# Optimization experiments

Hardware: AMD Instinct MI355X
Metric: run time of the kernel (lower is better)

## Reference

```python
import jax, jax.numpy as jnp
import numpy as np

N = 50000   # nodes
E = 800000  # edges (avg degree 16)
G = 32      # graphs in batch
IN = 128; HID = 64; H = 2; C = 16
NEG_SLOPE = 0.2
BN_EPS = 1e-5


def setup_inputs() -> dict:
    key = jax.random.key(0)
    ks = jax.random.split(key, 16)
    def rn(k, shape, scale=0.1):
        return jax.random.normal(k, shape, jnp.float32) * scale
    return {
        "feat": jax.random.normal(ks[0], (N, IN), jnp.float32),
        "W0": rn(ks[1], (IN, H * HID)),
        "attn0": rn(ks[2], (H, HID)),
        "W1": rn(ks[3], (H * HID, H * HID)),
        "attn1": rn(ks[4], (H, HID)),
        "W2": rn(ks[5], (H * HID, H * HID)),
        "attn2": rn(ks[6], (H, HID)),
        "Wf": rn(ks[7], (H * HID, H * C)),
        "attnf": rn(ks[8], (H, C)),
        "mlp_w1": rn(ks[9], (C, C)),
        "mlp_gamma": jnp.ones((C,), jnp.float32),
        "mlp_beta": jnp.zeros((C,), jnp.float32),
        "mlp_w2": rn(ks[10], (C, C)),
        "src": jax.random.randint(ks[11], (E,), 0, N, jnp.int32),
        "dst": jax.random.randint(ks[12], (E,), 0, N, jnp.int32),
        "node_graph": jnp.sort(jax.random.randint(ks[13], (N,), 0, G, jnp.int32)),
        "num_graphs": G,
    }


def gatv2_layer(h, src, dst, W, attn, act):
    """DGL GATv2Conv with share_weights=True, bias=False, residual=False."""
    n = h.shape[0]
    nh, d = attn.shape
    z = (h @ W).reshape(n, nh, d)                      # [N,H,D]
    zs = z[src]                                        # [E,H,D] gather (src)
    e = jax.nn.leaky_relu(zs + z[dst], NEG_SLOPE)      # [E,H,D]
    score = jnp.einsum('ehd,hd->eh', e, attn)          # [E,H]
    # edge softmax over incoming edges of dst (shift-invariant max trick)
    m = jax.lax.stop_gradient(jax.ops.segment_max(score, dst, num_segments=n))
    a = jnp.exp(score - m[dst])
    denom = jax.ops.segment_sum(a, dst, num_segments=n)[dst]
    alpha = a / jnp.where(denom == 0, 1.0, denom)      # [E,H]
    out = jax.ops.segment_sum(alpha[..., None] * zs, dst, num_segments=n)  # [N,H,D]
    return act(out) if act is not None else out


def reference(feat, W0, attn0, W1, attn1, W2, attn2, Wf, attnf,
              mlp_w1, mlp_gamma, mlp_beta, mlp_w2,
              src, dst, node_graph, num_graphs):
    relu = jax.nn.relu
    n = feat.shape[0]
    h = gatv2_layer(feat, src, dst, W0, attn0, relu).reshape(n, -1)
    h = gatv2_layer(h, src, dst, W1, attn1, relu).reshape(n, -1)
    h = gatv2_layer(h, src, dst, W2, attn2, relu).reshape(n, -1)
    logits = gatv2_layer(h, src, dst, Wf, attnf, None).mean(axis=1)  # [N,C]
    pooled = jax.ops.segment_sum(logits, node_graph, num_segments=num_graphs)  # [G,C]
    # MLP: relu(batchnorm(lin0(x))) -> lin1 (training-mode batch stats, biased var)
    h1 = pooled @ mlp_w1
    mu = h1.mean(axis=0)
    var = h1.var(axis=0)
    h1 = (h1 - mu) / jnp.sqrt(var + BN_EPS) * mlp_gamma + mlp_beta
    out = relu(h1) @ mlp_w2
    return jax.nn.log_softmax(out, axis=-1)
```

## Files before the change

### kernel.cpp

```cpp
#include <hip/hip_runtime.h>
#include <hip/hip_bf16.h>
#include <hip/hip_fp16.h>
#include <math.h>

#define NN 50000
#define EE 800000
#define GG 32
#define HD 64
#define NHEAD 2
#define CCLS 16
#define NEG_SLOPE 0.2f
#define BN_EPS 1e-5f
#define LOG2E 1.4426950408889634f
#define STRIDE 64

typedef unsigned int u32;
typedef _Float16 hv2 __attribute__((ext_vector_type(2)));
typedef __fp16   cv2 __attribute__((ext_vector_type(2)));

__device__ __forceinline__ hv2 bch2(u32 u) { union { u32 u; hv2 h; } c; c.u = u; return c.h; }
__device__ __forceinline__ u32 pkrtz(float a, float b) {
    cv2 r = __builtin_amdgcn_cvt_pkrtz(a, b);
    union { cv2 h; u32 u; } c; c.h = r; return c.u;
}
__device__ __forceinline__ hv2 h2max(hv2 a, hv2 b) {
    return __builtin_elementwise_max(a, b);
}
__device__ __forceinline__ float fdot2(hv2 a, hv2 b, float c) {
#if __has_builtin(__builtin_amdgcn_fdot2)
    union { hv2 h; cv2 c2; } ua, ub;
    ua.h = a; ub.h = b;
    return __builtin_amdgcn_fdot2(ua.c2, ub.c2, c, false);
#else
    return fmaf((float)a[0], (float)b[0], fmaf((float)a[1], (float)b[1], c));
#endif
}


template<int KOUT, int RPT, bool F16IN>
__device__ __forceinline__ void gemm_body(const void* __restrict__ hv,
                                          const float* __restrict__ W,
                                          u32* __restrict__ z, int n, int blk) {
    constexpr int CT = KOUT / 8;
    constexpr int RT = 256 / CT;
    constexpr int BR = RT * RPT;
    constexpr int WSTR = KOUT + 4;
    __shared__ __align__(16) u32 WpD[64 * WSTR];
    __shared__ __align__(16) uint4 hsU4[BR * 17];
    int t = threadIdx.x;
    int row0 = blk * BR;

    for (int i = t; i < 64 * (KOUT / 4); i += 256) {
        int k2 = i / (KOUT / 4), cq = i % (KOUT / 4);
        float4 wa = ((const float4*)W)[(2 * k2) * (KOUT / 4) + cq];
        float4 wb = ((const float4*)W)[(2 * k2 + 1) * (KOUT / 4) + cq];
        uint4 d;
        d.x = pkrtz(wa.x, wb.x); d.y = pkrtz(wa.y, wb.y);
        d.z = pkrtz(wa.z, wb.z); d.w = pkrtz(wa.w, wb.w);
        ((uint4*)&WpD[k2 * WSTR])[cq] = d;
    }
    for (int i = t; i < BR * 16; i += 256) {
        int r = i >> 4, c16 = i & 15;
        int gr = row0 + r;
        uint4 u = {0, 0, 0, 0};
        if (gr < n) {
            if (F16IN) {
                u = ((const uint4*)hv)[(size_t)gr * 16 + c16];
            } else {
                float4 f0 = ((const float4*)hv)[(size_t)gr * 32 + 2 * c16];
                float4 f1 = ((const float4*)hv)[(size_t)gr * 32 + 2 * c16 + 1];
                u.x = pkrtz(f0.x, f0.y); u.y = pkrtz(f0.z, f0.w);
                u.z = pkrtz(f1.x, f1.y); u.w = pkrtz(f1.z, f1.w);
            }
        }
        hsU4[r * 17 + c16] = u;
    }
    __syncthreads();

    int tc = t % CT, tr = t / CT;
    float acc[RPT][8];
    #pragma unroll
    for (int i = 0; i < RPT; i++)
        #pragma unroll
        for (int c = 0; c < 8; c++) acc[i][c] = 0.f;

    for (int kq = 0; kq < 16; kq++) {
        uint4 a4[RPT];
        #pragma unroll
        for (int i = 0; i < RPT; i++) a4[i] = hsU4[(tr * RPT + i) * 17 + kq];
        #pragma unroll
        for (int j = 0; j < 4; j++) {
            const u32* wrow = &WpD[(4 * kq + j) * WSTR + tc * 8];
            uint4 wa = *(const uint4*)wrow;
            uint4 wb = *(const uint4*)(wrow + 4);
            u32 wd[8] = {wa.x, wa.y, wa.z, wa.w, wb.x, wb.y, wb.z, wb.w};
            #pragma unroll
            for (int i = 0; i < RPT; i++) {
                u32 av[4] = {a4[i].x, a4[i].y, a4[i].z, a4[i].w};
                hv2 a2 = bch2(av[j]);
                #pragma unroll
                for (int c = 0; c < 8; c++)
                    acc[i][c] = fdot2(a2, bch2(wd[c]), acc[i][c]);
            }
        }
    }
    #pragma unroll
    for (int i = 0; i < RPT; i++) {
        int gr = row0 + tr * RPT + i;
        if (gr < n) {
            uint4 p;
            p.x = pkrtz(acc[i][0], acc[i][1]);
            p.y = pkrtz(acc[i][2], acc[i][3]);
            p.z = pkrtz(acc[i][4], acc[i][5]);
            p.w = pkrtz(acc[i][6], acc[i][7]);
            ((uint4*)z)[(size_t)gr * (KOUT / 8) + tc] = p;
        }
    }
}

template<int KOUT, int RPT, bool F16IN>
__global__ __launch_bounds__(256) void gemm_kernel(const void* __restrict__ hv,
                                                   const float* __restrict__ W,
                                                   u32* __restrict__ z, int n) {
    gemm_body<KOUT, RPT, F16IN>(hv, W, z, n, blockIdx.x);
}


#define GB0 782
#define SB0 782

__global__ __launch_bounds__(256) void gemm0_scatter_kernel(const float* __restrict__ feat,
                                                            const float* __restrict__ W,
                                                            u32* __restrict__ z,
                                                            const int* __restrict__ src,
                                                            const int* __restrict__ dst,
                                                            int* __restrict__ cursor,
                                                            int* __restrict__ csr_src) {
    if (blockIdx.x < GB0) {
        gemm_body<128, 4, false>(feat, W, z, NN, blockIdx.x);
    } else {
        int b = blockIdx.x - GB0;
        int e0 = b * 1024 + threadIdx.x;
        #pragma unroll
        for (int q = 0; q < 4; q++) {
            int e = e0 + q * 256;
            if (e < EE) {
                int d = dst[e];
                int s = src[e];
                int p = atomicAdd(&cursor[d], 1);
                csr_src[d * STRIDE + p] = s;
            }
        }
    }
}


__global__ __launch_bounds__(256) void edge_kernel(const u32* __restrict__ z,
                                                   const float* __restrict__ attn,
                                                   const int* __restrict__ cursor,
                                                   const int* __restrict__ csr_src,
                                                   u32* __restrict__ out, int n) {
    int wave = blockIdx.x * 4 + (threadIdx.x >> 6);
    int lane = threadIdx.x & 63;
    if (wave >= n) return;
    int i = wave;
    int slot = lane >> 3;
    int q8 = lane & 7;
    const uint4* zr = (const uint4*)z;

    size_t rowi = (size_t)i * 16 + q8 * 2;
    uint4 zua = zr[rowi], zub = zr[rowi + 1];
    hv2 zd[8] = {bch2(zua.x), bch2(zua.y), bch2(zua.z), bch2(zua.w),
                 bch2(zub.x), bch2(zub.y), bch2(zub.z), bch2(zub.w)};
    const float4* af = (const float4*)attn;
    float4 a0 = af[q8 * 4 + 0], a1 = af[q8 * 4 + 1];
    float4 a2 = af[q8 * 4 + 2], a3 = af[q8 * 4 + 3];
    hv2 ah[8] = {bch2(pkrtz(a0.x * LOG2E, a0.y * LOG2E)),
                 bch2(pkrtz(a0.z * LOG2E, a0.w * LOG2E)),
                 bch2(pkrtz(a1.x * LOG2E, a1.y * LOG2E)),
                 bch2(pkrtz(a1.z * LOG2E, a1.w * LOG2E)),
                 bch2(pkrtz(a2.x * LOG2E, a2.y * LOG2E)),
                 bch2(pkrtz(a2.z * LOG2E, a2.w * LOG2E)),
                 bch2(pkrtz(a3.x * LOG2E, a3.y * LOG2E)),
                 bch2(pkrtz(a3.z * LOG2E, a3.w * LOG2E))};
    const hv2 slope2 = {(_Float16)NEG_SLOPE, (_Float16)NEG_SLOPE};

    int deg = cursor[i];
    const int* ep = csr_src + i * STRIDE;

    float s = 0.f;
    float accf[16];
    #pragma unroll
    for (int j = 0; j < 16; j++) accf[j] = 0.f;

    for (int k = 0; k < deg; k += 8) {
        int kk = k + slot;
        bool valid = kk < deg;
        int sid = valid ? ep[kk] : i;
        size_t rs = (size_t)sid * 16 + q8 * 2;
        uint4 sa = zr[rs], sb = zr[rs + 1];
        hv2 zs[8] = {bch2(sa.x), bch2(sa.y), bch2(sa.z), bch2(sa.w),
                     bch2(sb.x), bch2(sb.y), bch2(sb.z), bch2(sb.w)};
        float sc = 0.f;
        #pragma unroll
        for (int j = 0; j < 8; j++) {
            hv2 x = zs[j] + zd[j];
            x = h2max(x, x * slope2);
            sc = fdot2(x, ah[j], sc);
        }
        sc += __shfl_xor(sc, 2, 64);
        sc += __shfl_xor(sc, 1, 64);
        float p = valid ? exp2f(sc) : 0.f;
        s += p;
        #pragma unroll
        for (int j = 0; j < 8; j++) {
            accf[2 * j]     = fmaf(p, (float)zs[j][0], accf[2 * j]);
            accf[2 * j + 1] = fmaf(p, (float)zs[j][1], accf[2 * j + 1]);
        }
    }

    #pragma unroll
    for (int off = 8; off <= 32; off <<= 1) {
        s += __shfl_xor(s, off, 64);
        #pragma unroll
        for (int j = 0; j < 16; j++) accf[j] += __shfl_xor(accf[j], off, 64);
    }

    if (slot == 0) {
        float inv = s > 0.f ? 1.f / s : 0.f;
        float o[16];
        #pragma unroll
        for (int j = 0; j < 16; j++) o[j] = fmaxf(accf[j] * inv, 0.f);
        uint4 pa, pb;
        pa.x = pkrtz(o[0], o[1]);   pa.y = pkrtz(o[2], o[3]);
        pa.z = pkrtz(o[4], o[5]);   pa.w = pkrtz(o[6], o[7]);
        pb.x = pkrtz(o[8], o[9]);   pb.y = pkrtz(o[10], o[11]);
        pb.z = pkrtz(o[12], o[13]); pb.w = pkrtz(o[14], o[15]);
        ((uint4*)out)[rowi] = pa;
        ((uint4*)out)[rowi + 1] = pb;
    }
}


__global__ __launch_bounds__(256) void edge_final_kernel(const u32* __restrict__ z,
                                                         const float* __restrict__ attn,
                                                         const int* __restrict__ cursor,
                                                         const int* __restrict__ csr_src,
                                                         float* __restrict__ logits, int n) {
    int wave = blockIdx.x * 4 + (threadIdx.x >> 6);
    int lane = threadIdx.x & 63;
    int iv = wave * 2 + (lane >> 5);
    bool mine = iv < n;
    int i = mine ? iv : (n - 1);
    int hl = lane & 31;
    int j = hl >> 3;
    int d8 = hl & 7;
    const uint2* zr = (const uint2*)z;
    uint2 zu = zr[(size_t)i * 8 + d8];
    hv2 zd0 = bch2(zu.x), zd1 = bch2(zu.y);
    float4 av = ((const float4*)attn)[d8];
    hv2 ah0 = bch2(pkrtz(av.x * LOG2E, av.y * LOG2E));
    hv2 ah1 = bch2(pkrtz(av.z * LOG2E, av.w * LOG2E));
    const hv2 slope2 = {(_Float16)NEG_SLOPE, (_Float16)NEG_SLOPE};
    int deg = cursor[i];
    const int* ep = csr_src + i * STRIDE;

    float s = 0.f;
    float accf[4] = {0.f, 0.f, 0.f, 0.f};
    for (int k = 0; k < deg; k += 4) {
        int kk = k + j;
        bool valid = kk < deg;
        int sid = valid ? ep[kk] : i;
        uint2 su = zr[(size_t)sid * 8 + d8];
        hv2 zs0 = bch2(su.x), zs1 = bch2(su.y);
        hv2 x;
        float sc = 0.f;
        x = zs0 + zd0; x = h2max(x, x * slope2); sc = fdot2(x, ah0, sc);
        x = zs1 + zd1; x = h2max(x, x * slope2); sc = fdot2(x, ah1, sc);
        sc += __shfl_xor(sc, 1, 64);
        sc += __shfl_xor(sc, 2, 64);
        float p = valid ? exp2f(sc) : 0.f;
        s += p;
        accf[0] = fmaf(p, (float)zs0[0], accf[0]);
        accf[1] = fmaf(p, (float)zs0[1], accf[1]);
        accf[2] = fmaf(p, (float)zs1[0], accf[2]);
        accf[3] = fmaf(p, (float)zs1[1], accf[3]);
    }
    #pragma unroll
    for (int off = 8; off <= 16; off <<= 1) {
        s += __shfl_xor(s, off, 64);
        #pragma unroll
        for (int jj = 0; jj < 4; jj++) accf[jj] += __shfl_xor(accf[jj], off, 64);
    }
    float inv = s > 0.f ? 1.f / s : 0.f;
    float4 o;
    o.x = accf[0] * inv; o.y = accf[1] * inv; o.z = accf[2] * inv; o.w = accf[3] * inv;
    o.x = 0.5f * (o.x + __shfl_xor(o.x, 4, 64));
    o.y = 0.5f * (o.y + __shfl_xor(o.y, 4, 64));
    o.z = 0.5f * (o.z + __shfl_xor(o.z, 4, 64));
    o.w = 0.5f * (o.w + __shfl_xor(o.w, 4, 64));
    if (mine && j == 0 && (hl & 4) == 0)
        ((float4*)logits)[i * 4 + (hl & 3)] = o;
}


__global__ __launch_bounds__(256) void pool_kernel(const float* __restrict__ logits,
                                                   const int* __restrict__ node_graph,
                                                   float* __restrict__ pooled) {
    int t = threadIdx.x;
    int c = t & 15;
    int ci = t >> 4;
    int start = blockIdx.x * 1024 + ci * 64;
    float acc = 0.f;
    int gcur = -1;
    for (int j = 0; j < 64; j++) {
        int node = start + j;
        if (node >= NN) break;
        int g = node_graph[node];
        if (g != gcur) {
            if (gcur >= 0) atomicAdd(&pooled[gcur * 16 + c], acc);
            gcur = g; acc = 0.f;
        }
        acc += logits[node * 16 + c];
    }
    if (gcur >= 0) atomicAdd(&pooled[gcur * 16 + c], acc);
}


__global__ __launch_bounds__(512) void mlp_kernel(const float* __restrict__ pooled,
                                                  const float* __restrict__ w1,
                                                  const float* __restrict__ gamma,
                                                  const float* __restrict__ beta,
                                                  const float* __restrict__ w2,
                                                  float* __restrict__ out) {
    __shared__ float P[GG * CCLS], H1[GG * CCLS], H2[GG * CCLS], O[GG * CCLS];
    __shared__ float mu[CCLS], rstd[CCLS], rowm[GG], rowl[GG];
    int t = threadIdx.x;
    int r = t >> 4, c = t & 15;
    if (t < GG * CCLS) P[t] = pooled[t];
    __syncthreads();
    if (t < GG * CCLS) {
        float s = 0.f;
        for (int k = 0; k < 16; k++) s += P[r * 16 + k] * w1[k * 16 + c];
        H1[t] = s;
    }
    __syncthreads();
    if (t < CCLS) {
        float s = 0.f;
        for (int rr = 0; rr < GG; rr++) s += H1[rr * 16 + t];
        float mn = s / GG;
        float s2 = 0.f;
        for (int rr = 0; rr < GG; rr++) { float d = H1[rr * 16 + t] - mn; s2 += d * d; }
        mu[t] = mn; rstd[t] = rsqrtf(s2 / GG + BN_EPS);
    }
    __syncthreads();
    if (t < GG * CCLS) {
        float v = (H1[t] - mu[c]) * rstd[c] * gamma[c] + beta[c];
        H2[t] = fmaxf(v, 0.f);
    }
    __syncthreads();
    if (t < GG * CCLS) {
        float s = 0.f;
        for (int k = 0; k < 16; k++) s += H2[r * 16 + k] * w2[k * 16 + c];
        O[t] = s;
    }
    __syncthreads();
    if (t < GG) {
        float mx = -INFINITY;
        for (int k = 0; k < 16; k++) mx = fmaxf(mx, O[t * 16 + k]);
        float l = 0.f;
        for (int k = 0; k < 16; k++) l += __expf(O[t * 16 + k] - mx);
        rowm[t] = mx; rowl[t] = logf(l);
    }
    __syncthreads();
    if (t < GG * CCLS) out[t] = O[t] - rowm[r] - rowl[r];
}


extern "C" void kernel_launch(void* const* d_in, const int* in_sizes, int n_in,
                              void* d_out, int out_size, void* d_ws, size_t ws_size,
                              hipStream_t stream) {
    const float* feat     = (const float*)d_in[0];
    const float* W0       = (const float*)d_in[1];
    const float* attn0    = (const float*)d_in[2];
    const float* W1       = (const float*)d_in[3];
    const float* attn1    = (const float*)d_in[4];
    const float* W2       = (const float*)d_in[5];
    const float* attn2    = (const float*)d_in[6];
    const float* Wf       = (const float*)d_in[7];
    const float* attnf    = (const float*)d_in[8];
    const float* mlp_w1   = (const float*)d_in[9];
    const float* mlp_g    = (const float*)d_in[10];
    const float* mlp_b    = (const float*)d_in[11];
    const float* mlp_w2   = (const float*)d_in[12];
    const int*   src      = (const int*)d_in[13];
    const int*   dst      = (const int*)d_in[14];
    const int*   ngraph   = (const int*)d_in[15];
    float* out = (float*)d_out;

    char* ws = (char*)d_ws;
    size_t off = 0;
    auto alloc = [&](size_t bytes) {
        void* p = ws + off;
        off = (off + bytes + 255) & ~(size_t)255;
        return p;
    };
    u32* z      = (u32*)alloc((size_t)NN * 64 * sizeof(u32));
    u32* hb0    = (u32*)alloc((size_t)NN * 64 * sizeof(u32));
    u32* hb1    = (u32*)alloc((size_t)NN * 64 * sizeof(u32));
    float* logits = (float*)alloc((size_t)NN * 16 * sizeof(float));
    float* pooled = (float*)alloc(GG * CCLS * sizeof(float));
    int* cursor   = (int*)alloc(NN * sizeof(int));
    int* csr_src  = (int*)alloc((size_t)NN * STRIDE * sizeof(int));

    hipMemsetAsync(cursor, 0, NN * sizeof(int), stream);
    hipMemsetAsync(pooled, 0, GG * CCLS * sizeof(float), stream);

    int edge_grid = (NN + 3) / 4;
    int edgef_grid = (NN + 7) / 8;
    int gemm_grid = (NN + 63) / 64;

    gemm0_scatter_kernel<<<GB0 + SB0, 256, 0, stream>>>(feat, W0, z, src, dst,
                                                        cursor, csr_src);
    edge_kernel<<<edge_grid, 256, 0, stream>>>(z, attn0, cursor, csr_src, hb0, NN);

    gemm_kernel<128, 4, true><<<gemm_grid, 256, 0, stream>>>(hb0, W1, z, NN);
    edge_kernel<<<edge_grid, 256, 0, stream>>>(z, attn1, cursor, csr_src, hb1, NN);

    gemm_kernel<128, 4, true><<<gemm_grid, 256, 0, stream>>>(hb1, W2, z, NN);
    edge_kernel<<<edge_grid, 256, 0, stream>>>(z, attn2, cursor, csr_src, hb0, NN);

    gemm_kernel<32, 1, true><<<gemm_grid, 256, 0, stream>>>(hb0, Wf, z, NN);
    edge_final_kernel<<<edgef_grid, 256, 0, stream>>>(z, attnf, cursor, csr_src, logits, NN);

    pool_kernel<<<(NN + 1023) / 1024, 256, 0, stream>>>(logits, ngraph, pooled);
    mlp_kernel<<<1, 512, 0, stream>>>(pooled, mlp_w1, mlp_g, mlp_b, mlp_w2, out);
}
```

Measured before the change: 427.2 us.

## Split gemm0/scatter kernels, pad weight LDS layout, prefetch next edge batch

Splits the fused first GEMM + CSR scatter kernel into two separate launches, and restructures the scatter to load all four dst/src pairs before issuing atomics. Pads the KOUT=128 weight tile in LDS with an extra 4-word gap every 32 words to reduce bank conflicts on the uint4 reads. In the edge kernel, the gather of the next batch of 8 neighbor rows is software-prefetched while the current batch is being computed, to hide gather latency at the cost of extra registers. Splitting the fused kernel removes the concurrency between the GEMM and the scatter and adds one launch.

```diff
diff --git a/kernel.cpp b/kernel.cpp
--- a/kernel.cpp
+++ b/kernel.cpp
@@ -37,6 +37,30 @@
 }
 
 
+__global__ __launch_bounds__(256) void scatter_kernel(const int* __restrict__ src,
+                                                      const int* __restrict__ dst,
+                                                      int* __restrict__ cursor,
+                                                      int* __restrict__ csr_src) {
+    int e0 = blockIdx.x * 1024 + threadIdx.x;
+    int d[4], s[4];
+    bool v[4];
+    #pragma unroll
+    for (int q = 0; q < 4; q++) {
+        int e = e0 + q * 256;
+        v[q] = e < EE;
+        d[q] = v[q] ? dst[e] : 0;
+        s[q] = v[q] ? src[e] : 0;
+    }
+    #pragma unroll
+    for (int q = 0; q < 4; q++) {
+        if (v[q]) {
+            int p = atomicAdd(&cursor[d[q]], 1);
+            csr_src[d[q] * STRIDE + p] = s[q];
+        }
+    }
+}
+
+
 template<int KOUT, int RPT, bool F16IN>
 __device__ __forceinline__ void gemm_body(const void* __restrict__ hv,
                                           const float* __restrict__ W,
@@ -44,7 +68,7 @@
     constexpr int CT = KOUT / 8;
     constexpr int RT = 256 / CT;
     constexpr int BR = RT * RPT;
-    constexpr int WSTR = KOUT + 4;
+    constexpr int WSTR = (KOUT == 128) ? 140 : (KOUT + 4);
     __shared__ __align__(16) u32 WpD[64 * WSTR];
     __shared__ __align__(16) uint4 hsU4[BR * 17];
     int t = threadIdx.x;
@@ -57,7 +81,7 @@
         uint4 d;
         d.x = pkrtz(wa.x, wb.x); d.y = pkrtz(wa.y, wb.y);
         d.z = pkrtz(wa.z, wb.z); d.w = pkrtz(wa.w, wb.w);
-        ((uint4*)&WpD[k2 * WSTR])[cq] = d;
+        *(uint4*)&WpD[k2 * WSTR + 4 * cq + ((cq >> 3) << 2)] = d;
     }
     for (int i = t; i < BR * 16; i += 256) {
         int r = i >> 4, c16 = i & 15;
@@ -90,7 +114,7 @@
         for (int i = 0; i < RPT; i++) a4[i] = hsU4[(tr * RPT + i) * 17 + kq];
         #pragma unroll
         for (int j = 0; j < 4; j++) {
-            const u32* wrow = &WpD[(4 * kq + j) * WSTR + tc * 8];
+            const u32* wrow = &WpD[(4 * kq + j) * WSTR + tc * 8 + ((tc >> 2) << 2)];
             uint4 wa = *(const uint4*)wrow;
             uint4 wb = *(const uint4*)(wrow + 4);
             u32 wd[8] = {wa.x, wa.y, wa.z, wa.w, wb.x, wb.y, wb.z, wb.w};
@@ -123,35 +147,6 @@
                                                    const float* __restrict__ W,
                                                    u32* __restrict__ z, int n) {
     gemm_body<KOUT, RPT, F16IN>(hv, W, z, n, blockIdx.x);
-}
-
-
-#define GB0 782
-#define SB0 782
-
-__global__ __launch_bounds__(256) void gemm0_scatter_kernel(const float* __restrict__ feat,
-                                                            const float* __restrict__ W,
-                                                            u32* __restrict__ z,
-                                                            const int* __restrict__ src,
-                                                            const int* __restrict__ dst,
-                                                            int* __restrict__ cursor,
-                                                            int* __restrict__ csr_src) {
-    if (blockIdx.x < GB0) {
-        gemm_body<128, 4, false>(feat, W, z, NN, blockIdx.x);
-    } else {
-        int b = blockIdx.x - GB0;
-        int e0 = b * 1024 + threadIdx.x;
-        #pragma unroll
-        for (int q = 0; q < 4; q++) {
-            int e = e0 + q * 256;
-            if (e < EE) {
-                int d = dst[e];
-                int s = src[e];
-                int p = atomicAdd(&cursor[d], 1);
-                csr_src[d * STRIDE + p] = s;
-            }
-        }
-    }
 }
 
 
@@ -193,12 +188,20 @@
     #pragma unroll
     for (int j = 0; j < 16; j++) accf[j] = 0.f;
 
+    bool valid = slot < deg;
+    int sid = valid ? ep[slot] : i;
+    size_t rs = (size_t)sid * 16 + q8 * 2;
+    uint4 sa = zr[rs], sb = zr[rs + 1];
+
     for (int k = 0; k < deg; k += 8) {
-        int kk = k + slot;
-        bool valid = kk < deg;
-        int sid = valid ? ep[kk] : i;
-        size_t rs = (size_t)sid * 16 + q8 * 2;
-        uint4 sa = zr[rs], sb = zr[rs + 1];
+        bool more = (k + 8) < deg;
+        bool v2 = (k + 8 + slot) < deg;
+        uint4 na, nb;
+        if (more) {
+            int sid2 = v2 ? ep[k + 8 + slot] : i;
+            size_t rs2 = (size_t)sid2 * 16 + q8 * 2;
+            na = zr[rs2]; nb = zr[rs2 + 1];
+        }
         hv2 zs[8] = {bch2(sa.x), bch2(sa.y), bch2(sa.z), bch2(sa.w),
                      bch2(sb.x), bch2(sb.y), bch2(sb.z), bch2(sb.w)};
         float sc = 0.f;
@@ -217,6 +220,7 @@
             accf[2 * j]     = fmaf(p, (float)zs[j][0], accf[2 * j]);
             accf[2 * j + 1] = fmaf(p, (float)zs[j][1], accf[2 * j + 1]);
         }
+        sa = na; sb = nb; valid = v2;
     }
 
     #pragma unroll
@@ -419,9 +423,10 @@
     int edge_grid = (NN + 3) / 4;
     int edgef_grid = (NN + 7) / 8;
     int gemm_grid = (NN + 63) / 64;
-
-    gemm0_scatter_kernel<<<GB0 + SB0, 256, 0, stream>>>(feat, W0, z, src, dst,
-                                                        cursor, csr_src);
+    int scat_grid = (EE + 1023) / 1024;
+
+    gemm_kernel<128, 4, false><<<gemm_grid, 256, 0, stream>>>(feat, W0, z, NN);
+    scatter_kernel<<<scat_grid, 256, 0, stream>>>(src, dst, cursor, csr_src);
     edge_kernel<<<edge_grid, 256, 0, stream>>>(z, attn0, cursor, csr_src, hb0, NN);
 
     gemm_kernel<128, 4, true><<<gemm_grid, 256, 0, stream>>>(hb0, W1, z, NN);
```

Result: slower. 447.3 us (+4.7%).
